# Kernel tuning notes

Hardware: AMD Instinct MI355X
Metric: run time of the kernel (lower is better)

Reference implementation:

```python
import jax, jax.numpy as jnp
import numpy as np

B, L, DM = 2, 2048, 2048
DI = 2 * DM          # d_inner = expand * d_model
N = 16               # d_state
K = 4                # d_conv
R = DM // 16         # dt_rank = ceil(d_model/16) = 128
FF = 8192            # intermediate_size
EPS = 1e-5


def _silu(x):
    return x * jax.nn.sigmoid(x)


def _ln(x, w, b):
    mu = jnp.mean(x, -1, keepdims=True)
    var = jnp.mean((x - mu) ** 2, -1, keepdims=True)
    return (x - mu) * jax.lax.rsqrt(var + EPS) * w + b


def setup_inputs() -> dict:
    key = jax.random.key(0)
    ks = jax.random.split(key, 8)

    def w(k, shape, fan_in):
        return jax.random.normal(k, shape, jnp.float32) / np.sqrt(fan_in).astype(np.float32)

    return {
        "hidden_states": jax.random.normal(ks[0], (B, L, DM), jnp.float32),
        "ln1_w": jnp.ones((DM,), jnp.float32),
        "ln1_b": jnp.zeros((DM,), jnp.float32),
        "W_in": w(ks[1], (2 * DI, DM), DM),      # in_proj (x and gate merged)
        "conv_w": w(ks[2], (DI, K), K),           # depthwise causal conv weights
        "conv_b": jnp.zeros((DI,), jnp.float32),
        "W_x": w(ks[3], (R + 2 * N, DI), DI),     # x_proj -> [dt_rank | B | C]
        "W_dt": w(ks[4], (DI, R), R),             # dt_proj (bias applied in scan)
        "b_dt": jnp.full((DI,), -2.0, jnp.float32),
        "A": -jnp.tile(jnp.arange(1.0, N + 1.0, dtype=jnp.float32), (DI, 1)),  # (DI, N)
        "Dp": jnp.ones((DI,), jnp.float32),
        "W_out": w(ks[5], (DM, DI), DI),
        "ln2_w": jnp.ones((DM,), jnp.float32),
        "ln2_b": jnp.zeros((DM,), jnp.float32),
        "W_fc1": w(ks[6], (2 * FF, DM), DM),      # GLU: [gate | y]
        "W_fc2": w(ks[7], (DM, FF), FF),
    }


def reference(hidden_states, ln1_w, ln1_b, W_in, conv_w, conv_b, W_x, W_dt, b_dt,
              A, Dp, W_out, ln2_w, ln2_b, W_fc1, W_fc2):
    # --- input layernorm + Phi4Mamba (prefill path: causal_conv1d_fn + selective_scan_fn) ---
    res = hidden_states
    x = _ln(hidden_states, ln1_w, ln1_b)

    xz = jnp.einsum('bld,ed->ble', x, W_in)           # (B, L, 2*DI)
    xs, gate = jnp.split(xz, 2, axis=-1)              # each (B, L, DI)

    # depthwise causal conv1d (width K) fused with silu
    xp = jnp.pad(xs, ((0, 0), (K - 1, 0), (0, 0)))
    conv = conv_b
    for k in range(K):
        conv = conv + xp[:, k:k + L, :] * conv_w[:, k]
    xs = _silu(conv)                                  # (B, L, DI)

    ssm = jnp.einsum('bld,ed->ble', xs, W_x)          # (B, L, R+2N)
    dt, Bm, Cm = ssm[..., :R], ssm[..., R:R + N], ssm[..., R + N:]
    delta = jax.nn.softplus(jnp.einsum('blr,dr->bld', dt, W_dt) + b_dt)  # (B, L, DI)

    def step(h, inp):
        d_t, b_t, c_t, x_t = inp                       # (B,DI),(B,N),(B,N),(B,DI)
        h = jnp.exp(d_t[..., None] * A) * h + (d_t * x_t)[..., None] * b_t[:, None, :]
        return h, jnp.einsum('bdn,bn->bd', h, c_t)

    h0 = jnp.zeros((B, DI, N), xs.dtype)
    _, ys = jax.lax.scan(step, h0, (delta.transpose(1, 0, 2), Bm.transpose(1, 0, 2),
                                    Cm.transpose(1, 0, 2), xs.transpose(1, 0, 2)))
    y = ys.transpose(1, 0, 2) + Dp * xs               # (B, L, DI)
    y = y * _silu(gate)                                # selective_scan z-gating
    attn_out = jnp.einsum('bld,ed->ble', y, W_out)    # (B, L, DM)

    hs = res + attn_out

    # --- post layernorm + GLU MLP ---
    res2 = hs
    x2 = _ln(hs, ln2_w, ln2_b)
    gy = jnp.einsum('bld,ed->ble', x2, W_fc1)         # (B, L, 2*FF)
    g, yy = jnp.split(gy, 2, axis=-1)
    mlp = jnp.einsum('blf,df->bld', yy * _silu(g), W_fc2)
    return res2 + mlp
```

## Files before the change

### kernel.cpp

```cpp
#include <hip/hip_runtime.h>
#include <hip/hip_bf16.h>

typedef unsigned short u16;
typedef unsigned int u32;

#define L_SEQ 2048
#define DMODEL 2048
#define DINNER 4096
#define NSTATE 16
#define MROWS 4096
#define CHUNK 32
#define NCHK  64

typedef __bf16 bf16x8 __attribute__((ext_vector_type(8)));
typedef float f32x4 __attribute__((ext_vector_type(4)));

__device__ __forceinline__ u16 f2bf(float f) {
    union { float f; u32 u; } v; v.f = f;
    u32 u = v.u;
    u32 r = (u + 0x7fffu + ((u >> 16) & 1u)) >> 16;
    return (u16)r;
}
__device__ __forceinline__ float bf2f(u16 h) {
    union { u32 u; float f; } v; v.u = ((u32)h) << 16;
    return v.f;
}

__device__ __forceinline__ void gload16(const void* g, void* l) {
    __builtin_amdgcn_global_load_lds((const __attribute__((address_space(1))) void*)g,
                                     (__attribute__((address_space(3))) void*)l, 16, 0, 0);
}

__global__ __launch_bounds__(256) void cvt_kernel(const float* __restrict__ src,
                                                  u16* __restrict__ dst, long nsrc) {
    long i = ((long)blockIdx.x * 256 + threadIdx.x) * 8;
    union { uint4 v; u16 u[8]; } o;
    if (i < nsrc) {
        f32x4 a = *(const f32x4*)(src + i);
        f32x4 b = *(const f32x4*)(src + i + 4);
#pragma unroll
        for (int j = 0; j < 4; ++j) { o.u[j] = f2bf(a[j]); o.u[4 + j] = f2bf(b[j]); }
    } else {
#pragma unroll
        for (int j = 0; j < 8; ++j) o.u[j] = 0;
    }
    *(uint4*)(dst + i) = o.v;
}

__global__ __launch_bounds__(256) void cvt_fc1_kernel(const float* __restrict__ src,
                                                      u16* __restrict__ dst) {
    long id = (long)blockIdx.x * 256 + threadIdx.x;
    int r = (int)(id >> 8);
    int c8 = (int)(id & 255) * 8;
    int g16 = r >> 5, k = r & 31;
    int sr = (k < 16) ? (g16 * 16 + k) : (8192 + g16 * 16 + (k - 16));
    const float* s = src + (long)sr * 2048 + c8;
    f32x4 a = *(const f32x4*)s;
    f32x4 b = *(const f32x4*)(s + 4);
    union { uint4 v; u16 u[8]; } o;
#pragma unroll
    for (int j = 0; j < 4; ++j) { o.u[j] = f2bf(a[j]); o.u[4 + j] = f2bf(b[j]); }
    *(uint4*)(dst + (long)r * 2048 + c8) = o.v;
}

__global__ __launch_bounds__(256) void ln_kernel(const float* __restrict__ in,
                                                 const float* __restrict__ w,
                                                 const float* __restrict__ b,
                                                 u16* __restrict__ out) {
    const long row = blockIdx.x;
    const float* x = in + row * DMODEL;
    const int t = threadIdx.x;
    f32x4 v0 = *(const f32x4*)(x + t * 8);
    f32x4 v1 = *(const f32x4*)(x + t * 8 + 4);
    float s = 0.f, sq = 0.f;
#pragma unroll
    for (int j = 0; j < 4; ++j) {
        s += v0[j] + v1[j];
        sq += v0[j] * v0[j] + v1[j] * v1[j];
    }
#pragma unroll
    for (int off = 32; off > 0; off >>= 1) {
        s += __shfl_down(s, off);
        sq += __shfl_down(sq, off);
    }
    __shared__ float red[8];
    __shared__ float stats[2];
    const int wid = t >> 6, lane = t & 63;
    if (lane == 0) { red[wid] = s; red[4 + wid] = sq; }
    __syncthreads();
    if (t == 0) {
        float S = red[0] + red[1] + red[2] + red[3];
        float Q = red[4] + red[5] + red[6] + red[7];
        float mu = S / (float)DMODEL;
        stats[0] = mu;
        stats[1] = rsqrtf(Q / (float)DMODEL - mu * mu + 1e-5f);
    }
    __syncthreads();
    float mu = stats[0], rstd = stats[1];
    union { uint4 v; u16 u[8]; } o;
#pragma unroll
    for (int j = 0; j < 8; ++j) {
        float xv = (j < 4) ? v0[j] : v1[j - 4];
        o.u[j] = f2bf((xv - mu) * rstd * w[t * 8 + j] + b[t * 8 + j]);
    }
    *(uint4*)(out + row * DMODEL + t * 8) = o.v;
}

__global__ __launch_bounds__(256) void reduce_ln_kernel(const float* __restrict__ p0,
                                                        const float* __restrict__ p1,
                                                        const float* __restrict__ add,
                                                        const float* __restrict__ w,
                                                        const float* __restrict__ b,
                                                        float* __restrict__ hs_out,
                                                        u16* __restrict__ ln_out) {
    const long row = blockIdx.x;
    const long base = row * DMODEL;
    const int t = threadIdx.x;
    f32x4 v0, v1;
    {
        f32x4 a0 = *(const f32x4*)(p0 + base + t * 8);
        f32x4 a1 = *(const f32x4*)(p0 + base + t * 8 + 4);
        f32x4 b0 = *(const f32x4*)(p1 + base + t * 8);
        f32x4 b1 = *(const f32x4*)(p1 + base + t * 8 + 4);
        f32x4 c0 = *(const f32x4*)(add + base + t * 8);
        f32x4 c1 = *(const f32x4*)(add + base + t * 8 + 4);
#pragma unroll
        for (int j = 0; j < 4; ++j) { v0[j] = a0[j] + b0[j] + c0[j]; v1[j] = a1[j] + b1[j] + c1[j]; }
    }
    *(f32x4*)(hs_out + base + t * 8) = v0;
    *(f32x4*)(hs_out + base + t * 8 + 4) = v1;
    float s = 0.f, sq = 0.f;
#pragma unroll
    for (int j = 0; j < 4; ++j) {
        s += v0[j] + v1[j];
        sq += v0[j] * v0[j] + v1[j] * v1[j];
    }
#pragma unroll
    for (int off = 32; off > 0; off >>= 1) {
        s += __shfl_down(s, off);
        sq += __shfl_down(sq, off);
    }
    __shared__ float red[8];
    __shared__ float stats[2];
    const int wid = t >> 6, lane = t & 63;
    if (lane == 0) { red[wid] = s; red[4 + wid] = sq; }
    __syncthreads();
    if (t == 0) {
        float S = red[0] + red[1] + red[2] + red[3];
        float Q = red[4] + red[5] + red[6] + red[7];
        float mu = S / (float)DMODEL;
        stats[0] = mu;
        stats[1] = rsqrtf(Q / (float)DMODEL - mu * mu + 1e-5f);
    }
    __syncthreads();
    float mu = stats[0], rstd = stats[1];
    union { uint4 v; u16 u[8]; } o;
#pragma unroll
    for (int j = 0; j < 8; ++j) {
        float xv = (j < 4) ? v0[j] : v1[j - 4];
        o.u[j] = f2bf((xv - mu) * rstd * w[t * 8 + j] + b[t * 8 + j]);
    }
    *(uint4*)(ln_out + base + t * 8) = o.v;
}

template <int MODE>
__global__ __launch_bounds__(256) void gemm_bt(const u16* __restrict__ A,
                                               const u16* __restrict__ W,
                                               float* __restrict__ Cf,
                                               u16* __restrict__ Cb,
                                               const float* __restrict__ addv,
                                               int M, int N, int K, int lda, int ldb) {
    __shared__ u16 As[128 * 64];
    __shared__ u16 Bs[128 * 64];
    const int tid = threadIdx.x;
    const int wid = tid >> 6;
    const int lane = tid & 63;
    const int m0 = blockIdx.y << 7;
    const int n0 = blockIdx.x << 7;
    const long koff = (long)blockIdx.z * K;
    const long zoff = (long)blockIdx.z * M * N;
    const int wr = (wid >> 1) << 6;
    const int wc = (wid & 1) << 6;
    const int l15 = lane & 15;
    const int lhi = lane >> 4;

    f32x4 acc[4][4];
#pragma unroll
    for (int i = 0; i < 4; ++i)
#pragma unroll
        for (int j = 0; j < 4; ++j) acc[i][j] = (f32x4){0.f, 0.f, 0.f, 0.f};

    const int srow = (wid << 3) + (lane >> 3);
    const int scol = (lane & 7) << 3;

    const u16* aBase = A + (long)(m0 + srow) * lda + scol + koff;
    const u16* bBase = W + (long)(n0 + srow) * (long)ldb + scol + koff;

    for (int k0 = 0; k0 < K; k0 += 64) {
#pragma unroll
        for (int i = 0; i < 4; ++i) {
            gload16(aBase + (long)(i * 32) * lda + k0, &As[((i << 5) + (wid << 3)) << 6]);
            gload16(bBase + (long)(i * 32) * ldb + k0, &Bs[((i << 5) + (wid << 3)) << 6]);
        }
        __syncthreads();
#pragma unroll
        for (int kk = 0; kk < 64; kk += 32) {
            bf16x8 af[4], bfr[4];
#pragma unroll
            for (int i = 0; i < 4; ++i)
                af[i] = *(const bf16x8*)&As[((wr + (i << 4) + l15) << 6) + kk + (lhi << 3)];
#pragma unroll
            for (int j = 0; j < 4; ++j)
                bfr[j] = *(const bf16x8*)&Bs[((wc + (j << 4) + l15) << 6) + kk + (lhi << 3)];
#pragma unroll
            for (int i = 0; i < 4; ++i)
#pragma unroll
                for (int j = 0; j < 4; ++j)
                    acc[i][j] = __builtin_amdgcn_mfma_f32_16x16x32_bf16(af[i], bfr[j], acc[i][j], 0, 0, 0);
        }
        __syncthreads();
    }

#pragma unroll
    for (int i = 0; i < 4; ++i) {
#pragma unroll
        for (int j = 0; j < 4; ++j) {
#pragma unroll
            for (int r = 0; r < 4; ++r) {
                int row = m0 + wr + (i << 4) + (lhi << 2) + r;
                int col = n0 + wc + (j << 4) + l15;
                long idx = (long)row * N + col;
                float v = acc[i][j][r];
                if (MODE == 1) Cb[idx] = f2bf(v);
                else Cf[zoff + idx] = v;
            }
        }
    }
}

template <int MODE>
__global__ __launch_bounds__(512, 2) void gemm8(const u16* __restrict__ A,
                                                const u16* __restrict__ W,
                                                float* __restrict__ Cf,
                                                u16* __restrict__ Cb,
                                                int M, int N, int K, int lda, int ldb) {
    __shared__ u16 lds[4][2][256 * 32];
    const int tid = threadIdx.x;
    const int wid = tid >> 6;
    const int lane = tid & 63;
    const int wr = wid >> 2;
    const int wc = wid & 3;
    const int l15 = lane & 15;
    const int lhi = lane >> 4;
    const int sw = (l15 >> 1) & 3;
    const long koff = (long)blockIdx.z * K;
    const long zoff = (long)blockIdx.z * M * N;

    const int nwg = gridDim.x * gridDim.y;
    const int flat = blockIdx.y * gridDim.x + blockIdx.x;
    const int q8 = nwg >> 3, r8 = nwg & 7;
    const int xcd = flat & 7, lid = flat >> 3;
    const int swz = (xcd < r8 ? xcd * (q8 + 1) : r8 * (q8 + 1) + (xcd - r8) * q8) + lid;
    const int m0 = (swz % gridDim.y) << 8;
    const int n0 = (swz / gridDim.y) << 8;

    const int srow = lane >> 2;
    const int gc16 = (lane & 3) ^ ((lane >> 3) & 3);

    f32x4 acc[8][4];
#pragma unroll
    for (int i = 0; i < 8; ++i)
#pragma unroll
        for (int j = 0; j < 4; ++j) acc[i][j] = (f32x4){0.f, 0.f, 0.f, 0.f};

#define STAGE_A(t, j)                                                                              \
    gload16(A + (long)(m0 + (j) * 128 + wid * 16 + srow) * lda + koff + (long)(t) * 32 + gc16 * 8, \
            &lds[(t) & 3][0][((j) * 128 + wid * 16) * 32])
#define STAGE_B(t, j)                                                                              \
    gload16(W + (long)(n0 + (j) * 128 + wid * 16 + srow) * (long)ldb + koff + (long)(t) * 32 + gc16 * 8, \
            &lds[(t) & 3][1][((j) * 128 + wid * 16) * 32])
#define RD_A(buf, f0)  *(const bf16x8*)&lds[buf][0][((wr * 128 + (f0) * 16 + l15)) * 32 + ((lhi ^ sw) << 3)]
#define RD_B(buf, f0)  *(const bf16x8*)&lds[buf][1][((wc * 64 + (f0) * 16 + l15)) * 32 + ((lhi ^ sw) << 3)]
#define MFMA16(ab)                                                                                  \
    __builtin_amdgcn_s_setprio(1);                                                                  \
    _Pragma("unroll")                                                                               \
    for (int ii = 0; ii < 4; ++ii)                                                                  \
        _Pragma("unroll")                                                                           \
        for (int jj = 0; jj < 4; ++jj)                                                              \
            acc[(ab) + ii][jj] = __builtin_amdgcn_mfma_f32_16x16x32_bf16(a[ii], bb[jj], acc[(ab) + ii][jj], 0, 0, 0); \
    __builtin_amdgcn_s_setprio(0);

    STAGE_A(0, 0); STAGE_A(0, 1); STAGE_B(0, 0); STAGE_B(0, 1);
    STAGE_A(1, 0); STAGE_A(1, 1); STAGE_B(1, 0); STAGE_B(1, 1);
    asm volatile("s_waitcnt vmcnt(4)" ::: "memory");
    __builtin_amdgcn_s_barrier();
    __builtin_amdgcn_sched_barrier(0);

    const int nt2 = K >> 6;
    for (int i = 0; i < nt2; ++i) {
        const int t0 = 2 * i;
        const int b0 = t0 & 3, b1 = (t0 + 1) & 3;
        const bool more = (i + 1 < nt2);
        bf16x8 a[4], bb[4];
#pragma unroll
        for (int f = 0; f < 4; ++f) a[f] = RD_A(b0, f);
#pragma unroll
        for (int f = 0; f < 4; ++f) bb[f] = RD_B(b0, f);
        if (more) { STAGE_A(t0 + 2, 0); STAGE_A(t0 + 2, 1); }
        MFMA16(0)
#pragma unroll
        for (int f = 0; f < 4; ++f) a[f] = RD_A(b0, f + 4);
        if (more) { STAGE_B(t0 + 2, 0); STAGE_B(t0 + 2, 1); }
        MFMA16(4)
        if (more) { asm volatile("s_waitcnt vmcnt(4)" ::: "memory"); }
        else      { asm volatile("s_waitcnt vmcnt(0)" ::: "memory"); }
        __builtin_amdgcn_s_barrier();
        __builtin_amdgcn_sched_barrier(0);
#pragma unroll
        for (int f = 0; f < 4; ++f) a[f] = RD_A(b1, f);
#pragma unroll
        for (int f = 0; f < 4; ++f) bb[f] = RD_B(b1, f);
        if (more) { STAGE_A(t0 + 3, 0); STAGE_A(t0 + 3, 1); }
        MFMA16(0)
#pragma unroll
        for (int f = 0; f < 4; ++f) a[f] = RD_A(b1, f + 4);
        if (more) { STAGE_B(t0 + 3, 0); STAGE_B(t0 + 3, 1); }
        MFMA16(4)
        if (more) {
            asm volatile("s_waitcnt vmcnt(4)" ::: "memory");
            __builtin_amdgcn_s_barrier();
            __builtin_amdgcn_sched_barrier(0);
        }
    }
#undef STAGE_A
#undef STAGE_B
#undef RD_A
#undef RD_B
#undef MFMA16

    if (MODE == 3) {
#pragma unroll
        for (int i = 0; i < 8; ++i) {
#pragma unroll
            for (int jp = 0; jp < 2; ++jp) {
                const int j = 2 * jp;
#pragma unroll
                for (int r = 0; r < 4; ++r) {
                    int row = m0 + wr * 128 + i * 16 + lhi * 4 + r;
                    int f = ((n0 + wc * 64) >> 1) + jp * 16 + l15;
                    float g = acc[i][j][r];
                    float yv = acc[i][j + 1][r];
                    Cb[(long)row * (N >> 1) + f] = f2bf(yv * (g / (1.f + __expf(-g))));
                }
            }
        }
    } else {
#pragma unroll
        for (int i = 0; i < 8; ++i) {
#pragma unroll
            for (int j = 0; j < 4; ++j) {
#pragma unroll
                for (int r = 0; r < 4; ++r) {
                    int row = m0 + wr * 128 + i * 16 + lhi * 4 + r;
                    int col = n0 + wc * 64 + j * 16 + l15;
                    long idx = (long)row * N + col;
                    if (MODE == 1) Cb[idx] = f2bf(acc[i][j][r]);
                    else Cf[zoff + idx] = acc[i][j][r];
                }
            }
        }
    }
}

__global__ __launch_bounds__(256) void reduce_add_kernel(const float* __restrict__ p0,
                                                         const float* __restrict__ p1,
                                                         const float* __restrict__ add,
                                                         float* __restrict__ out) {
    long i = ((long)blockIdx.x * 256 + threadIdx.x) * 4;
    f32x4 a = *(const f32x4*)(p0 + i);
    f32x4 b = *(const f32x4*)(p1 + i);
    f32x4 c = *(const f32x4*)(add + i);
    f32x4 o;
#pragma unroll
    for (int j = 0; j < 4; ++j) o[j] = a[j] + b[j] + c[j];
    *(f32x4*)(out + i) = o;
}

__global__ __launch_bounds__(256) void reduce4_bf16_kernel(const float* __restrict__ p,
                                                           u16* __restrict__ outb) {
    long i = ((long)blockIdx.x * 256 + threadIdx.x) * 4;
    const long S = 4096L * 256;
    f32x4 a = *(const f32x4*)(p + i);
    f32x4 b = *(const f32x4*)(p + S + i);
    f32x4 c = *(const f32x4*)(p + 2 * S + i);
    f32x4 d = *(const f32x4*)(p + 3 * S + i);
    union { uint2 v; u16 u[4]; } o;
#pragma unroll
    for (int j = 0; j < 4; ++j) o.u[j] = f2bf(a[j] + b[j] + c[j] + d[j]);
    *(uint2*)(outb + i) = o.v;
}

__global__ __launch_bounds__(256) void conv_silu_kernel(const u16* __restrict__ xz,
                                                        const float* __restrict__ cw,
                                                        const float* __restrict__ cb,
                                                        u16* __restrict__ act_out) {
    const int d0 = (blockIdx.x * 256 + threadIdx.x) * 8;
    const int bl = blockIdx.y;
    const int l = bl & (L_SEQ - 1);
    float acc[8];
    float wt[8][4];
#pragma unroll
    for (int j = 0; j < 8; ++j) {
        f32x4 wj = *(const f32x4*)(cw + (d0 + j) * 4);
        wt[j][0] = wj[0]; wt[j][1] = wj[1]; wt[j][2] = wj[2]; wt[j][3] = wj[3];
        acc[j] = cb[d0 + j];
    }
#pragma unroll
    for (int k = 0; k < 4; ++k) {
        int ls = l + k - 3;
        if (ls >= 0) {
            union { uint4 v; u16 u[8]; } xv;
            xv.v = *(const uint4*)(xz + (long)(bl + k - 3) * (2 * DINNER) + d0);
#pragma unroll
            for (int j = 0; j < 8; ++j) acc[j] = fmaf(bf2f(xv.u[j]), wt[j][k], acc[j]);
        }
    }
    union { uint4 v; u16 u[8]; } ob;
#pragma unroll
    for (int j = 0; j < 8; ++j) {
        float c = acc[j];
        ob.u[j] = f2bf(c / (1.f + __expf(-c)));
    }
    *(uint4*)(act_out + (long)bl * DINNER + d0) = ob.v;
}

__global__ __launch_bounds__(256) void scan1_kernel(float* __restrict__ dpre,
                                                    const u16* __restrict__ xs,
                                                    const u16* __restrict__ ssmb,
                                                    const float* __restrict__ Am,
                                                    const float* __restrict__ bdt,
                                                    float* __restrict__ hend,
                                                    float* __restrict__ sumd) {
    const int d = blockIdx.x * 256 + threadIdx.x;
    const int c = blockIdx.y;
    const int b = blockIdx.z;
    float a2[NSTATE];
#pragma unroll
    for (int n = 0; n < NSTATE; ++n) a2[n] = Am[d * NSTATE + n] * 1.4426950408889634f;
    float h[NSTATE];
#pragma unroll
    for (int n = 0; n < NSTATE; ++n) h[n] = 0.f;
    const float bd = bdt[d];
    float sd = 0.f;
    const long base = (long)b * L_SEQ + (long)c * CHUNK;
    for (int i = 0; i < CHUNK; ++i) {
        const long row = base + i;
        float dpv = dpre[row * DINNER + d] + bd;
        float delta = (dpv > 20.f) ? dpv : log1pf(__expf(dpv));
        dpre[row * DINNER + d] = delta;
        sd += delta;
        float dx = delta * bf2f(xs[row * DINNER + d]);
        const u16* sb = ssmb + row * 256;
#pragma unroll
        for (int n = 0; n < NSTATE; ++n)
            h[n] = __builtin_amdgcn_exp2f(delta * a2[n]) * h[n] + dx * bf2f(sb[128 + n]);
    }
    float* hb = hend + ((long)(b * NCHK + c) * DINNER + d) * NSTATE;
#pragma unroll
    for (int n = 0; n < NSTATE; n += 4)
        *(f32x4*)(hb + n) = (f32x4){h[n], h[n + 1], h[n + 2], h[n + 3]};
    sumd[(long)(b * NCHK + c) * DINNER + d] = sd;
}

__global__ __launch_bounds__(256) void scan2_kernel(float* __restrict__ hend,
                                                    const float* __restrict__ sumd,
                                                    const float* __restrict__ Am) {
    const long idx = (long)blockIdx.x * 256 + threadIdx.x;
    const int n = (int)(idx & 15);
    const int d = (int)((idx >> 4) & (DINNER - 1));
    const int b = (int)(idx >> 16);
    const float a2 = Am[d * NSTATE + n] * 1.4426950408889634f;
    float carry = 0.f;
    for (int c = 0; c < NCHK; ++c) {
        const long soff = (long)(b * NCHK + c) * DINNER + d;
        const long hoff = soff * NSTATE + n;
        float he = hend[hoff];
        float P = __builtin_amdgcn_exp2f(a2 * sumd[soff]);
        hend[hoff] = carry;
        carry = he + P * carry;
    }
}

__global__ __launch_bounds__(256) void scan3_kernel(const float* __restrict__ delta_,
                                                    const u16* __restrict__ xs,
                                                    const u16* __restrict__ ssmb,
                                                    const u16* __restrict__ xz,
                                                    const float* __restrict__ Am,
                                                    const float* __restrict__ Dp,
                                                    const float* __restrict__ hinit,
                                                    u16* __restrict__ yb) {
    const int d = blockIdx.x * 256 + threadIdx.x;
    const int c = blockIdx.y;
    const int b = blockIdx.z;
    float a2[NSTATE];
#pragma unroll
    for (int n = 0; n < NSTATE; ++n) a2[n] = Am[d * NSTATE + n] * 1.4426950408889634f;
    float h[NSTATE];
    const float* hb = hinit + ((long)(b * NCHK + c) * DINNER + d) * NSTATE;
#pragma unroll
    for (int n = 0; n < NSTATE; n += 4) {
        f32x4 hv = *(const f32x4*)(hb + n);
        h[n] = hv[0]; h[n + 1] = hv[1]; h[n + 2] = hv[2]; h[n + 3] = hv[3];
    }
    const float dp = Dp[d];
    const long base = (long)b * L_SEQ + (long)c * CHUNK;
    for (int i = 0; i < CHUNK; ++i) {
        const long row = base + i;
        float delta = delta_[row * DINNER + d];
        float xt = bf2f(xs[row * DINNER + d]);
        float dx = delta * xt;
        const u16* sb = ssmb + row * 256;
        float y = 0.f;
#pragma unroll
        for (int n = 0; n < NSTATE; ++n) {
            float Bn = bf2f(sb[128 + n]);
            float Cn = bf2f(sb[144 + n]);
            h[n] = __builtin_amdgcn_exp2f(delta * a2[n]) * h[n] + dx * Bn;
            y = fmaf(h[n], Cn, y);
        }
        float g = bf2f(xz[row * (2 * DINNER) + DINNER + d]);
        float yv = (y + dp * xt) * (g / (1.f + __expf(-g)));
        yb[row * DINNER + d] = f2bf(yv);
    }
}

extern "C" void kernel_launch(void* const* d_in, const int* in_sizes, int n_in,
                              void* d_out, int out_size, void* d_ws, size_t ws_size,
                              hipStream_t stream) {
    const float* hidden = (const float*)d_in[0];
    const float* ln1w   = (const float*)d_in[1];
    const float* ln1b   = (const float*)d_in[2];
    const float* W_in   = (const float*)d_in[3];
    const float* conv_w = (const float*)d_in[4];
    const float* conv_b = (const float*)d_in[5];
    const float* W_x    = (const float*)d_in[6];
    const float* W_dt   = (const float*)d_in[7];
    const float* b_dt   = (const float*)d_in[8];
    const float* Amat   = (const float*)d_in[9];
    const float* Dp     = (const float*)d_in[10];
    const float* W_out  = (const float*)d_in[11];
    const float* ln2w   = (const float*)d_in[12];
    const float* ln2b   = (const float*)d_in[13];
    const float* W_fc1  = (const float*)d_in[14];
    const float* W_fc2  = (const float*)d_in[15];
    float* out = (float*)d_out;

    char* ws = (char*)d_ws;
    const size_t SZ67 = 67108864;
    u16*   ACT   = (u16*)(ws);
    u16*   WB    = (u16*)(ws + SZ67);
    u16*   XZ    = (u16*)(ws + 2 * SZ67);
    float* DELTA = (float*)(ws + 4 * SZ67);
    u16*   SSMB  = (u16*)(ws + 5 * SZ67);
    float* HS    = (float*)(ws + 5 * SZ67 + 2097152);
    float* HEND  = (float*)WB;
    float* SUMD  = (float*)(ws + SZ67 + 33554432);
    float* PART2 = (float*)(ws + SZ67 + 37748736);
    float* PART  = DELTA;

    ln_kernel<<<MROWS, 256, 0, stream>>>(hidden, ln1w, ln1b, ACT);
    cvt_kernel<<<(int)((8192L * 2048) / 2048), 256, 0, stream>>>(W_in, WB, 8192L * 2048);
    gemm8<1><<<dim3(8192 / 256, MROWS / 256), 512, 0, stream>>>(ACT, WB, nullptr, XZ,
                                                                MROWS, 8192, 2048, 2048, 2048);
    conv_silu_kernel<<<dim3(2, MROWS), 256, 0, stream>>>(XZ, conv_w, conv_b, ACT);
    cvt_kernel<<<(int)((256L * 4096) / 2048), 256, 0, stream>>>(W_x, WB, 160L * 4096);
    gemm_bt<0><<<dim3(2, 32, 4), 256, 0, stream>>>(ACT, WB, PART2, nullptr, nullptr,
                                                   MROWS, 256, 1024, 4096, 4096);
    reduce4_bf16_kernel<<<1024, 256, 0, stream>>>(PART2, SSMB);
    cvt_kernel<<<(int)((4096L * 128) / 2048), 256, 0, stream>>>(W_dt, WB, 4096L * 128);
    gemm8<0><<<dim3(4096 / 256, MROWS / 256), 512, 0, stream>>>(SSMB, WB, DELTA, nullptr,
                                                                MROWS, 4096, 128, 256, 128);
    scan1_kernel<<<dim3(DINNER / 256, NCHK, 2), 256, 0, stream>>>(DELTA, ACT, SSMB, Amat, b_dt,
                                                                  HEND, SUMD);
    scan2_kernel<<<(2 * DINNER * NSTATE) / 256, 256, 0, stream>>>(HEND, SUMD, Amat);
    scan3_kernel<<<dim3(DINNER / 256, NCHK, 2), 256, 0, stream>>>(DELTA, ACT, SSMB, XZ, Amat, Dp,
                                                                  HEND, ACT);
    cvt_kernel<<<(int)((2048L * 4096) / 2048), 256, 0, stream>>>(W_out, WB, 2048L * 4096);
    gemm8<0><<<dim3(2048 / 256, MROWS / 256, 2), 512, 0, stream>>>(ACT, WB, PART, nullptr,
                                                                   MROWS, 2048, 2048, 4096, 4096);
    reduce_ln_kernel<<<MROWS, 256, 0, stream>>>(PART, PART + 4096L * 2048, hidden,
                                                ln2w, ln2b, HS, ACT);
    cvt_fc1_kernel<<<16384, 256, 0, stream>>>(W_fc1, WB);
    gemm8<3><<<dim3(16384 / 256, MROWS / 256), 512, 0, stream>>>(ACT, WB, nullptr, XZ,
                                                                 MROWS, 16384, 2048, 2048, 2048);
    cvt_kernel<<<(int)((2048L * 8192) / 2048), 256, 0, stream>>>(W_fc2, WB, 2048L * 8192);
    gemm8<0><<<dim3(2048 / 256, MROWS / 256, 2), 512, 0, stream>>>(XZ, WB, PART, nullptr,
                                                                   MROWS, 2048, 4096, 8192, 8192);
    reduce_add_kernel<<<(int)((4096L * 2048) / 1024), 256, 0, stream>>>(PART, PART + 4096L * 2048,
                                                                        HS, out);
}
```

Baseline: 1.001 ms.

## Store delta in bf16 and add barrier-synchronised MFMA phases in gemm8 loop

The dt_proj GEMM now writes its pre-activation as bf16 (MODE 1) instead of fp32, and the scan kernels read and write delta as bf16. This halves delta memory traffic across the gemm, scan1 and scan3 at the cost of lower precision in the softplus input and the stored delta. Separately, the main gemm8 K-loop gains extra workgroup barriers and explicit lgkmcnt(0) waits around each MFMA block, so waves run in lockstep phases. The extra barriers could add stalls to every GEMM.

```diff
diff --git a/kernel.cpp b/kernel.cpp
--- a/kernel.cpp
+++ b/kernel.cpp
@@ -281,6 +281,7 @@
             &lds[(t) & 3][1][((j) * 128 + wid * 16) * 32])
 #define RD_A(buf, f0)  *(const bf16x8*)&lds[buf][0][((wr * 128 + (f0) * 16 + l15)) * 32 + ((lhi ^ sw) << 3)]
 #define RD_B(buf, f0)  *(const bf16x8*)&lds[buf][1][((wc * 64 + (f0) * 16 + l15)) * 32 + ((lhi ^ sw) << 3)]
+#define LGKM0_SGB  asm volatile("s_waitcnt lgkmcnt(0)" ::: "memory"); __builtin_amdgcn_sched_barrier(0);
 #define MFMA16(ab)                                                                                  \
     __builtin_amdgcn_s_setprio(1);                                                                  \
     _Pragma("unroll")                                                                               \
@@ -307,10 +308,15 @@
 #pragma unroll
         for (int f = 0; f < 4; ++f) bb[f] = RD_B(b0, f);
         if (more) { STAGE_A(t0 + 2, 0); STAGE_A(t0 + 2, 1); }
+        __builtin_amdgcn_s_barrier();
+        LGKM0_SGB
         MFMA16(0)
+        __builtin_amdgcn_s_barrier();
 #pragma unroll
         for (int f = 0; f < 4; ++f) a[f] = RD_A(b0, f + 4);
         if (more) { STAGE_B(t0 + 2, 0); STAGE_B(t0 + 2, 1); }
+        __builtin_amdgcn_s_barrier();
+        LGKM0_SGB
         MFMA16(4)
         if (more) { asm volatile("s_waitcnt vmcnt(4)" ::: "memory"); }
         else      { asm volatile("s_waitcnt vmcnt(0)" ::: "memory"); }
@@ -321,21 +327,26 @@
 #pragma unroll
         for (int f = 0; f < 4; ++f) bb[f] = RD_B(b1, f);
         if (more) { STAGE_A(t0 + 3, 0); STAGE_A(t0 + 3, 1); }
+        __builtin_amdgcn_s_barrier();
+        LGKM0_SGB
         MFMA16(0)
+        __builtin_amdgcn_s_barrier();
 #pragma unroll
         for (int f = 0; f < 4; ++f) a[f] = RD_A(b1, f + 4);
         if (more) { STAGE_B(t0 + 3, 0); STAGE_B(t0 + 3, 1); }
+        __builtin_amdgcn_s_barrier();
+        LGKM0_SGB
         MFMA16(4)
-        if (more) {
-            asm volatile("s_waitcnt vmcnt(4)" ::: "memory");
-            __builtin_amdgcn_s_barrier();
-            __builtin_amdgcn_sched_barrier(0);
-        }
+        if (more) { asm volatile("s_waitcnt vmcnt(4)" ::: "memory"); }
+        else      { asm volatile("s_waitcnt vmcnt(0)" ::: "memory"); }
+        __builtin_amdgcn_s_barrier();
+        __builtin_amdgcn_sched_barrier(0);
     }
 #undef STAGE_A
 #undef STAGE_B
 #undef RD_A
 #undef RD_B
+#undef LGKM0_SGB
 #undef MFMA16
 
     if (MODE == 3) {
@@ -434,7 +445,7 @@
     *(uint4*)(act_out + (long)bl * DINNER + d0) = ob.v;
 }
 
-__global__ __launch_bounds__(256) void scan1_kernel(float* __restrict__ dpre,
+__global__ __launch_bounds__(256) void scan1_kernel(u16* __restrict__ dpre,
                                                     const u16* __restrict__ xs,
                                                     const u16* __restrict__ ssmb,
                                                     const float* __restrict__ Am,
@@ -455,9 +466,9 @@
     const long base = (long)b * L_SEQ + (long)c * CHUNK;
     for (int i = 0; i < CHUNK; ++i) {
         const long row = base + i;
-        float dpv = dpre[row * DINNER + d] + bd;
+        float dpv = bf2f(dpre[row * DINNER + d]) + bd;
         float delta = (dpv > 20.f) ? dpv : log1pf(__expf(dpv));
-        dpre[row * DINNER + d] = delta;
+        dpre[row * DINNER + d] = f2bf(delta);
         sd += delta;
         float dx = delta * bf2f(xs[row * DINNER + d]);
         const u16* sb = ssmb + row * 256;
@@ -491,7 +502,7 @@
     }
 }
 
-__global__ __launch_bounds__(256) void scan3_kernel(const float* __restrict__ delta_,
+__global__ __launch_bounds__(256) void scan3_kernel(const u16* __restrict__ delta_,
                                                     const u16* __restrict__ xs,
                                                     const u16* __restrict__ ssmb,
                                                     const u16* __restrict__ xz,
@@ -516,7 +527,7 @@
     const long base = (long)b * L_SEQ + (long)c * CHUNK;
     for (int i = 0; i < CHUNK; ++i) {
         const long row = base + i;
-        float delta = delta_[row * DINNER + d];
+        float delta = bf2f(delta_[row * DINNER + d]);
         float xt = bf2f(xs[row * DINNER + d]);
         float dx = delta * xt;
         const u16* sb = ssmb + row * 256;
@@ -560,13 +571,13 @@
     u16*   ACT   = (u16*)(ws);
     u16*   WB    = (u16*)(ws + SZ67);
     u16*   XZ    = (u16*)(ws + 2 * SZ67);
-    float* DELTA = (float*)(ws + 4 * SZ67);
+    u16*   DELTAB= (u16*)(ws + 4 * SZ67);
     u16*   SSMB  = (u16*)(ws + 5 * SZ67);
     float* HS    = (float*)(ws + 5 * SZ67 + 2097152);
     float* HEND  = (float*)WB;
     float* SUMD  = (float*)(ws + SZ67 + 33554432);
     float* PART2 = (float*)(ws + SZ67 + 37748736);
-    float* PART  = DELTA;
+    float* PART  = (float*)(ws + 4 * SZ67);
 
     ln_kernel<<<MROWS, 256, 0, stream>>>(hidden, ln1w, ln1b, ACT);
     cvt_kernel<<<(int)((8192L * 2048) / 2048), 256, 0, stream>>>(W_in, WB, 8192L * 2048);
@@ -578,12 +589,12 @@
                                                    MROWS, 256, 1024, 4096, 4096);
     reduce4_bf16_kernel<<<1024, 256, 0, stream>>>(PART2, SSMB);
     cvt_kernel<<<(int)((4096L * 128) / 2048), 256, 0, stream>>>(W_dt, WB, 4096L * 128);
-    gemm8<0><<<dim3(4096 / 256, MROWS / 256), 512, 0, stream>>>(SSMB, WB, DELTA, nullptr,
+    gemm8<1><<<dim3(4096 / 256, MROWS / 256), 512, 0, stream>>>(SSMB, WB, nullptr, DELTAB,
                                                                 MROWS, 4096, 128, 256, 128);
-    scan1_kernel<<<dim3(DINNER / 256, NCHK, 2), 256, 0, stream>>>(DELTA, ACT, SSMB, Amat, b_dt,
+    scan1_kernel<<<dim3(DINNER / 256, NCHK, 2), 256, 0, stream>>>(DELTAB, ACT, SSMB, Amat, b_dt,
                                                                   HEND, SUMD);
     scan2_kernel<<<(2 * DINNER * NSTATE) / 256, 256, 0, stream>>>(HEND, SUMD, Amat);
-    scan3_kernel<<<dim3(DINNER / 256, NCHK, 2), 256, 0, stream>>>(DELTA, ACT, SSMB, XZ, Amat, Dp,
+    scan3_kernel<<<dim3(DINNER / 256, NCHK, 2), 256, 0, stream>>>(DELTAB, ACT, SSMB, XZ, Amat, Dp,
                                                                   HEND, ACT);
     cvt_kernel<<<(int)((2048L * 4096) / 2048), 256, 0, stream>>>(W_out, WB, 2048L * 4096);
     gemm8<0><<<dim3(2048 / 256, MROWS / 256, 2), 512, 0, stream>>>(ACT, WB, PART, nullptr,
```

Result: slower. 1.035 ms (+3.4%).
